# Optimization experiments

Measured on AMD Instinct MI355X. Metric: run time of the kernel, lower is better.

The kernel has to match this reference:

```python
import jax, jax.numpy as jnp
import numpy as np

B, C, H, W = 8, 256, 64, 64
OUT, K = 256, 3
OG = 1
STRIDE, PAD, DIL = 1, 1, 1
K2 = K * K


def setup_inputs() -> dict:
    key = jax.random.key(0)
    ks = jax.random.split(key, 5)
    x = jax.random.normal(ks[0], (B, C, H, W), jnp.float32)
    # main deform-conv weight [out, in//groups, k, k]
    weight = jax.random.normal(ks[1], (OUT, C, K, K), jnp.float32) * (1.0 / np.sqrt(C * K2))
    bias = jax.random.normal(ks[2], (OUT,), jnp.float32) * 0.01
    # param_generator: 3x3 conv -> 3*OG*K*K channels (oh, ow, mask)
    pg_w = jax.random.normal(ks[3], (3 * OG * K2, C, 3, 3), jnp.float32) * 0.01
    pg_b = jax.random.normal(ks[4], (3 * OG * K2,), jnp.float32) * 0.01
    return {"x": x, "weight": weight, "bias": bias, "pg_w": pg_w, "pg_b": pg_b}


def _conv3x3(x, w, b):
    y = jax.lax.conv_general_dilated(
        x, w, (1, 1), [(1, 1), (1, 1)],
        dimension_numbers=("NCHW", "OIHW", "NCHW"))
    return y + b[None, :, None, None]


def _bilinear_gather(img, py, px):
    # img [B,C,H,W]; py,px [B,K2,Ho,Wo] -> [B,C,K2,Ho,Wo]
    # Zero padding outside the image (torchvision deform_conv2d semantics).
    Hh, Ww = img.shape[2], img.shape[3]
    y0 = jnp.floor(py)
    x0 = jnp.floor(px)
    dy = py - y0
    dx = px - x0
    imgf = img.reshape(img.shape[0], img.shape[1], Hh * Ww)
    out = jnp.zeros((img.shape[0], img.shape[1]) + py.shape[1:], img.dtype)
    corners = (
        (0, 0, (1 - dy) * (1 - dx)),
        (0, 1, (1 - dy) * dx),
        (1, 0, dy * (1 - dx)),
        (1, 1, dy * dx),
    )
    for oy, ox, wgt in corners:
        yy = y0 + oy
        xx = x0 + ox
        valid = (yy >= 0) & (yy < Hh) & (xx >= 0) & (xx < Ww)
        yi = jnp.clip(yy, 0, Hh - 1).astype(jnp.int32)
        xi = jnp.clip(xx, 0, Ww - 1).astype(jnp.int32)
        idx = yi * Ww + xi  # [B,K2,Ho,Wo]
        g = jax.vmap(lambda im, ix: jnp.take(im, ix.reshape(-1), axis=1))(imgf, idx)
        g = g.reshape(img.shape[0], img.shape[1], *idx.shape[1:])
        out = out + g * (wgt * valid)[:, None]
    return out


def _deform_conv2d(x, weight, bias, pg_w, pg_b):
    Bn = x.shape[0]
    Hi, Wi = x.shape[2], x.shape[3]
    Ho = (Hi + 2 * PAD - DIL * (K - 1) - 1) // STRIDE + 1
    Wo = (Wi + 2 * PAD - DIL * (K - 1) - 1) // STRIDE + 1
    params = _conv3x3(x, pg_w, pg_b)  # [B, 3*OG*K2, H, W]
    oh, ow, mask = jnp.split(params, 3, axis=1)
    offset = jnp.concatenate([oh, ow], axis=1)  # [B, 2*OG*K2, Ho, Wo]
    mask = jax.nn.sigmoid(mask)                  # [B, OG*K2, Ho, Wo]
    # torchvision layout: channel = ((og*K2 + k)*2 + {y,x})
    off = offset.reshape(Bn, OG, K2, 2, Ho, Wo)
    dy = off[:, :, :, 0].reshape(Bn, K2, Ho, Wo)  # OG == 1
    dx = off[:, :, :, 1].reshape(Bn, K2, Ho, Wo)
    hy = jnp.arange(Ho, dtype=x.dtype) * STRIDE - PAD
    wx = jnp.arange(Wo, dtype=x.dtype) * STRIDE - PAD
    ky, kx = jnp.meshgrid(jnp.arange(K), jnp.arange(K), indexing="ij")
    base_y = hy[None, :, None] + (ky.reshape(-1) * DIL).astype(x.dtype)[:, None, None]  # [K2,Ho,1]
    base_x = wx[None, None, :] + (kx.reshape(-1) * DIL).astype(x.dtype)[:, None, None]  # [K2,1,Wo]
    py = dy + base_y[None]  # [B,K2,Ho,Wo]
    px = dx + base_x[None]
    sampled = _bilinear_gather(x, py, px)          # [B,C,K2,Ho,Wo]
    sampled = sampled * mask[:, None]              # modulation (OG=1)
    out = jnp.einsum("bckhw,ock->bohw", sampled, weight.reshape(OUT, C, K2))
    return out + bias[None, :, None, None]


def reference(x, weight, bias, pg_w, pg_b):
    return _deform_conv2d(x, weight, bias, pg_w, pg_b)
```

## Files before the change

### kernel.cpp

```cpp
#include <hip/hip_runtime.h>
#include <math.h>

#define BQ   8
#define CIN  256
#define HH   64
#define WW   64
#define COUT 256
#define K2   9
#define PCH  27

#define PT     64
#define CCH    32
#define NCHUNK (CIN / CCH)
#define NSTEP  72
#define NSUB   24
#define SUBROW 104
#define PLANE  (HH * WW)

#define NXT    (BQ * HH * 4)
#define NPW    ((NSTEP * COUT * 4) / 256)
#define NPG    ((NSTEP * 32 * 4) / 256)
#define NPREP  (NXT + NPW + NPG)

typedef __attribute__((ext_vector_type(8))) short short8;
typedef __attribute__((ext_vector_type(4))) float f32x4;
typedef __attribute__((ext_vector_type(2))) float f32x2;

#define PIPE_BARRIER() do {                                   \
    asm volatile("s_waitcnt lgkmcnt(0)" ::: "memory");        \
    __builtin_amdgcn_s_barrier();                             \
    asm volatile("" ::: "memory");                            \
} while (0)

static __device__ __forceinline__ unsigned short f2bf(float f) {
    unsigned u = __builtin_bit_cast(unsigned, f);
    u += 0x7fff + ((u >> 16) & 1);
    return (unsigned short)(u >> 16);
}
static __device__ __forceinline__ f32x2 up2(unsigned u) {
    f32x2 r;
    r[0] = __builtin_bit_cast(float, u << 16);
    r[1] = __builtin_bit_cast(float, u & 0xffff0000u);
    return r;
}
static __device__ __forceinline__ unsigned cvtpk(float lo, float hi) {
    unsigned r;
    asm("v_cvt_pk_bf16_f32 %0, %1, %2" : "=v"(r) : "v"(lo), "v"(hi));
    return r;
}

__global__ __launch_bounds__(256) void k_prep(const float* __restrict__ x,
                                              unsigned short* __restrict__ xT,
                                              const float* __restrict__ w,
                                              unsigned short* __restrict__ wp,
                                              const float* __restrict__ pgw,
                                              unsigned short* __restrict__ wpg) {
    __shared__ float tile[64][65];
    int blk = blockIdx.x;

    if (blk < NXT) {
        int cc  = blk & 3;
        int y   = (blk >> 2) & 63;
        int b   = blk >> 8;
        int t   = threadIdx.x;
        int c0  = cc * 64;

        const float* xp = x + ((size_t)(b * CIN + c0) * HH + y) * WW;
#pragma unroll
        for (int r = 0; r < 16; ++r) {
            int cl = r * 4 + (t >> 6);
            int xx = t & 63;
            tile[cl][xx] = xp[(size_t)cl * PLANE + xx];
        }
        __syncthreads();
        unsigned short* op = xT + ((size_t)b * PLANE + (size_t)y * WW) * CIN + c0;
#pragma unroll
        for (int r = 0; r < 16; ++r) {
            int xx = r * 4 + (t >> 6);
            int cl = t & 63;
            op[(size_t)xx * CIN + cl] = f2bf(tile[cl][xx]);
        }
    } else if (blk < NXT + NPW) {
        int t = (blk - NXT) * 256 + threadIdx.x;
        int q = t & 3;
        int o = (t >> 2) & 255;
        int s = t >> 10;
        short8 sv;
#pragma unroll
        for (int j = 0; j < 8; ++j) {
            int pos   = s * 32 + q * 8 + j;
            int chunk = pos / (CCH * K2);
            int pl    = pos % (CCH * K2);
            int ktap  = pl >> 5;
            int c     = chunk * CCH + (pl & 31);
            sv[j] = (short)f2bf(w[(o * CIN + c) * K2 + ktap]);
        }
        *(short8*)(wp + (size_t)t * 8) = sv;
    } else {
        int t = (blk - NXT - NPW) * 256 + threadIdx.x;
        int q = t & 3;
        int o = (t >> 2) & 31;
        int s = t >> 7;
        short8 sv;
#pragma unroll
        for (int j = 0; j < 8; ++j) {
            int pos   = s * 32 + q * 8 + j;
            int chunk = pos / (CCH * K2);
            int pl    = pos % (CCH * K2);
            int ktap  = pl >> 5;
            int c     = chunk * CCH + (pl & 31);
            sv[j] = (o < PCH) ? (short)f2bf(pgw[(size_t)(o * CIN + c) * K2 + ktap]) : (short)0;
        }
        *(short8*)(wpg + (size_t)t * 8) = sv;
    }
}

__global__ __launch_bounds__(512, 2) void k_params(const unsigned short* __restrict__ xT,
                                                   const unsigned short* __restrict__ wpg,
                                                   const float* __restrict__ pgb,
                                                   float* __restrict__ pv) {
    __shared__ alignas(16) unsigned short s_rows[2][3][66][40];

    int blk = blockIdx.x;
    int swz = (blk & 7) * 64 + (blk >> 3);
    int b   = swz >> 6;
    int h   = swz & 63;
    int t   = threadIdx.x;

    int wv  = t >> 6;
    int lm  = t & 15;
    int lq  = (t >> 4) & 3;
    int ipg = wv >> 2;
    int rpg = wv & 3;

    const unsigned short* xTb = xT + (size_t)b * PLANE * CIN;

    if (t < 48) {
        int bufk = t >= 24;
        int tt  = t - bufk * 24;
        int ky  = tt >> 3;
        int rem = tt & 7;
        int col = (rem >> 2) * 65;
        int q   = rem & 3;
        uint4 z = make_uint4(0, 0, 0, 0);
        *(uint4*)&s_rows[bufk][ky][col][q * 8] = z;
    }
    __syncthreads();

    f32x4 accA = (f32x4){0.f, 0.f, 0.f, 0.f};
    f32x4 accB = (f32x4){0.f, 0.f, 0.f, 0.f};

    int pxm1 = t >> 3;
    int cgs  = (t & 7) * 4;

    uint2 R[3];
#pragma unroll
    for (int ky = 0; ky < 3; ++ky) {
        int y = h + ky - 1;
        R[ky] = make_uint2(0, 0);
        if ((unsigned)y < (unsigned)HH)
            R[ky] = *(const uint2*)(xTb + (size_t)(y * WW + pxm1) * CIN + cgs);
    }

    for (int ch = 0; ch < NCHUNK; ++ch) {
#pragma unroll
        for (int ky = 0; ky < 3; ++ky)
            *(uint2*)&s_rows[ch & 1][ky][pxm1 + 1][cgs] = R[ky];
        if (ch + 1 < NCHUNK) {
#pragma unroll
            for (int ky = 0; ky < 3; ++ky) {
                int y = h + ky - 1;
                R[ky] = make_uint2(0, 0);
                if ((unsigned)y < (unsigned)HH)
                    R[ky] = *(const uint2*)(xTb + (size_t)(y * WW + pxm1) * CIN
                                            + (ch + 1) * CCH + cgs);
            }
        }
        __syncthreads();
#pragma unroll
        for (int tap = 0; tap < K2; ++tap) {
            int ky = tap / 3, kx = tap % 3;
            short8 a  = *(const short8*)(wpg + (size_t)(ch * K2 + tap) * 32 * 32
                                         + (ipg * 16 + lm) * 32 + lq * 8);
            short8 bf = *(const short8*)&s_rows[ch & 1][ky][rpg * 16 + lm + kx][lq * 8];
            if (tap & 1)
                accB = __builtin_amdgcn_mfma_f32_16x16x32_bf16(a, bf, accB, 0, 0, 0);
            else
                accA = __builtin_amdgcn_mfma_f32_16x16x32_bf16(a, bf, accA, 0, 0, 0);
        }
    }

    f32x4 accpg = accA + accB;
    int px = rpg * 16 + lm;
#pragma unroll
    for (int rg = 0; rg < 4; ++rg) {
        int oc = ipg * 16 + lq * 4 + rg;
        if (oc < PCH)
            pv[((size_t)(b * PCH + oc) << 12) + h * WW + px] = accpg[rg] + pgb[oc];
    }
}

__global__ __launch_bounds__(512, 4) void k_fused(const unsigned short* __restrict__ xT,
                                                  const unsigned short* __restrict__ wp,
                                                  const float* __restrict__ pv,
                                                  const float* __restrict__ bias,
                                                  float* __restrict__ out) {
    __shared__ alignas(16) unsigned short s_samp[2][PT][SUBROW];
    __shared__ float4 s_wgt4[K2][PT];
    __shared__ int4   s_off4[K2][PT];

    int blk = blockIdx.x;
    int swz = (blk & 7) * 64 + (blk >> 3);
    int b   = swz >> 6;
    int h   = swz & 63;
    int t   = threadIdx.x;

    int gp = t >> 3;
    int cg = t & 7;
    int wv = t >> 6;
    int lm = t & 15;
    int lq = (t >> 4) & 3;

    const char* xTb = (const char*)xT + (size_t)b * PLANE * CIN * 2;

    const float* pvb = pv + ((size_t)(b * PCH) << 12) + h * WW;
    for (int e = t; e < K2 * PT; e += 512) {
        int k = e >> 6;
        int p = e & 63;
        float dy = pvb[(size_t)(2 * k) << 12 | (unsigned)p];
        float dx = pvb[(size_t)(2 * k + 1) << 12 | (unsigned)p];
        float mz = pvb[(size_t)(18 + k) << 12 | (unsigned)p];
        float m  = 1.f / (1.f + expf(-mz));

        float py = dy + (float)(h - 1 + k / 3);
        float px = dx + (float)(p - 1 + k % 3);
        float y0f = floorf(py), x0f = floorf(px);
        float fy = py - y0f,    fx = px - x0f;
        int iy0 = (int)y0f, ix0 = (int)x0f;
        int iy1 = iy0 + 1,  ix1 = ix0 + 1;
        bool vy0 = (unsigned)iy0 < (unsigned)HH;
        bool vy1 = (unsigned)iy1 < (unsigned)HH;
        bool vx0 = (unsigned)ix0 < (unsigned)WW;
        bool vx1 = (unsigned)ix1 < (unsigned)WW;

        float w00 = (1.f - fy) * (1.f - fx) * m; if (!(vy0 && vx0)) w00 = 0.f;
        float w01 = (1.f - fy) * fx         * m; if (!(vy0 && vx1)) w01 = 0.f;
        float w10 = fy         * (1.f - fx) * m; if (!(vy1 && vx0)) w10 = 0.f;
        float w11 = fy         * fx         * m; if (!(vy1 && vx1)) w11 = 0.f;

        int cy0 = min(max(iy0, 0), HH - 1), cy1 = min(max(iy1, 0), HH - 1);
        int cx0 = min(max(ix0, 0), WW - 1), cx1 = min(max(ix1, 0), WW - 1);

        s_wgt4[k][p] = make_float4(w00, w01, w10, w11);
        s_off4[k][p] = make_int4((cy0 * WW + cx0) * 512, (cy0 * WW + cx1) * 512,
                                 (cy1 * WW + cx0) * 512, (cy1 * WW + cx1) * 512);
    }
    __syncthreads();

    int ow = wv * 32;
    f32x4 acc[2][4];
#pragma unroll
    for (int i = 0; i < 2; ++i)
#pragma unroll
        for (int j = 0; j < 4; ++j) acc[i][j] = (f32x4){0.f, 0.f, 0.f, 0.f};

    uint2 G[3][4];
    {
#pragma unroll
        for (int j = 0; j < 3; ++j) {
            int4 ob = s_off4[j][gp];
            G[j][0] = *(const uint2*)(xTb + ob.x + cg * 8);
            G[j][1] = *(const uint2*)(xTb + ob.y + cg * 8);
            G[j][2] = *(const uint2*)(xTb + ob.z + cg * 8);
            G[j][3] = *(const uint2*)(xTb + ob.w + cg * 8);
        }
#pragma unroll
        for (int j = 0; j < 3; ++j) {
            float4 gw = s_wgt4[j][gp];
            f32x2 v01 = gw.x * up2(G[j][0].x) + gw.y * up2(G[j][1].x)
                      + gw.z * up2(G[j][2].x) + gw.w * up2(G[j][3].x);
            f32x2 v23 = gw.x * up2(G[j][0].y) + gw.y * up2(G[j][1].y)
                      + gw.z * up2(G[j][2].y) + gw.w * up2(G[j][3].y);
            uint2 pk;
            pk.x = cvtpk(v01[0], v01[1]);
            pk.y = cvtpk(v23[0], v23[1]);
            *(uint2*)&s_samp[0][gp][j * 32 + cg * 4] = pk;
        }
#pragma unroll
        for (int j = 0; j < 3; ++j) {
            int4 ob = s_off4[3 + j][gp];
            G[j][0] = *(const uint2*)(xTb + ob.x + cg * 8);
            G[j][1] = *(const uint2*)(xTb + ob.y + cg * 8);
            G[j][2] = *(const uint2*)(xTb + ob.z + cg * 8);
            G[j][3] = *(const uint2*)(xTb + ob.w + cg * 8);
        }
        PIPE_BARRIER();
    }

    short8 a0c = *(const short8*)(wp + (ow +  0 + lm) * 32 + lq * 8);
    short8 a1c = *(const short8*)(wp + (ow + 16 + lm) * 32 + lq * 8);
    for (int sc = 0; sc < NSUB; ++sc) {
        bool doC = (sc + 1 < NSUB);
        bool doL = (sc + 2 < NSUB);
        int t1 = ((sc + 1) % 3) * 3;
        int t2 = ((sc + 2) % 3) * 3;
        int c2 = ((sc + 2) / 3) * (CCH * 2) + cg * 8;
        unsigned short (*__restrict__ bc)[SUBROW] = s_samp[sc & 1];
        unsigned short (*__restrict__ bn)[SUBROW] = s_samp[(sc + 1) & 1];
#pragma unroll
        for (int sl = 0; sl < 3; ++sl) {
            short8 b0 = *(const short8*)&bc[ 0 + lm][sl * 32 + lq * 8];
            short8 b1 = *(const short8*)&bc[16 + lm][sl * 32 + lq * 8];
            short8 b2 = *(const short8*)&bc[32 + lm][sl * 32 + lq * 8];
            short8 b3 = *(const short8*)&bc[48 + lm][sl * 32 + lq * 8];
            int r = sc * 3 + sl + 1;
            short8 a0n = a0c, a1n = a1c;
            if (r < NSTEP) {
                const unsigned short* wrn = wp + (size_t)r * COUT * 32;
                a0n = *(const short8*)(wrn + (ow +  0 + lm) * 32 + lq * 8);
                a1n = *(const short8*)(wrn + (ow + 16 + lm) * 32 + lq * 8);
            }
            if (doC) {
                float4 gw = s_wgt4[t1 + sl][gp];
                f32x2 v01 = gw.x * up2(G[sl][0].x) + gw.y * up2(G[sl][1].x)
                          + gw.z * up2(G[sl][2].x) + gw.w * up2(G[sl][3].x);
                f32x2 v23 = gw.x * up2(G[sl][0].y) + gw.y * up2(G[sl][1].y)
                          + gw.z * up2(G[sl][2].y) + gw.w * up2(G[sl][3].y);
                uint2 pk;
                pk.x = cvtpk(v01[0], v01[1]);
                pk.y = cvtpk(v23[0], v23[1]);
                *(uint2*)&bn[gp][sl * 32 + cg * 4] = pk;
            }
            if (doL) {
                int4 ob = s_off4[t2 + sl][gp];
                G[sl][0] = *(const uint2*)(xTb + ob.x + c2);
                G[sl][1] = *(const uint2*)(xTb + ob.y + c2);
                G[sl][2] = *(const uint2*)(xTb + ob.z + c2);
                G[sl][3] = *(const uint2*)(xTb + ob.w + c2);
            }
            __builtin_amdgcn_s_setprio(1);
            acc[0][0] = __builtin_amdgcn_mfma_f32_16x16x32_bf16(a0c, b0, acc[0][0], 0, 0, 0);
            acc[0][1] = __builtin_amdgcn_mfma_f32_16x16x32_bf16(a0c, b1, acc[0][1], 0, 0, 0);
            acc[0][2] = __builtin_amdgcn_mfma_f32_16x16x32_bf16(a0c, b2, acc[0][2], 0, 0, 0);
            acc[0][3] = __builtin_amdgcn_mfma_f32_16x16x32_bf16(a0c, b3, acc[0][3], 0, 0, 0);
            acc[1][0] = __builtin_amdgcn_mfma_f32_16x16x32_bf16(a1c, b0, acc[1][0], 0, 0, 0);
            acc[1][1] = __builtin_amdgcn_mfma_f32_16x16x32_bf16(a1c, b1, acc[1][1], 0, 0, 0);
            acc[1][2] = __builtin_amdgcn_mfma_f32_16x16x32_bf16(a1c, b2, acc[1][2], 0, 0, 0);
            acc[1][3] = __builtin_amdgcn_mfma_f32_16x16x32_bf16(a1c, b3, acc[1][3], 0, 0, 0);
            __builtin_amdgcn_s_setprio(0);
            a0c = a0n; a1c = a1n;
        }
        PIPE_BARRIER();
    }

    float* op = out + ((size_t)b * COUT) * PLANE + h * WW;
#pragma unroll
    for (int i = 0; i < 2; ++i) {
        int o0 = ow + i * 16 + lq * 4;
        f32x4 bv = *(const f32x4*)(bias + o0);
#pragma unroll
        for (int rg = 0; rg < 4; ++rg) {
#pragma unroll
            for (int j = 0; j < 4; ++j)
                op[(size_t)(o0 + rg) * PLANE + j * 16 + lm] = acc[i][j][rg] + bv[rg];
        }
    }
}

extern "C" void kernel_launch(void* const* d_in, const int* in_sizes, int n_in,
                              void* d_out, int out_size, void* d_ws, size_t ws_size,
                              hipStream_t stream) {
    const float* x    = (const float*)d_in[0];
    const float* wgt  = (const float*)d_in[1];
    const float* bias = (const float*)d_in[2];
    const float* pgw  = (const float*)d_in[3];
    const float* pgb  = (const float*)d_in[4];
    float* out = (float*)d_out;

    const size_t WPK_B = (size_t)NSTEP * COUT * 32 * 2;
    const size_t WPG_B = (size_t)NSTEP * 32 * 32 * 2;
    const size_t XT_B  = (size_t)BQ * PLANE * CIN * 2;
    unsigned short* wpk = (unsigned short*)d_ws;
    unsigned short* wpg = (unsigned short*)((char*)d_ws + WPK_B);
    unsigned short* xT  = (unsigned short*)((char*)d_ws + WPK_B + WPG_B);
    float*          pv  = (float*)((char*)d_ws + WPK_B + WPG_B + XT_B);

    k_prep  <<<NPREP, 256, 0, stream>>>(x, xT, wgt, wpk, pgw, wpg);
    k_params<<<BQ * HH, 512, 0, stream>>>(xT, wpg, pgb, pv);
    k_fused <<<BQ * HH, 512, 0, stream>>>(xT, wpk, pv, bias, out);
}
```

Before: 111.0 us.

## Merge offset-param conv into prep kernel reading fp32 x; retile fused MFMA warps

The offset/mask parameter convolution now runs inside the prep kernel, alongside the transpose and weight-packing blocks, and reads fp32 x directly with on-the-fly bf16 conversion. This removes the dependency on the transposed xT buffer and lets param work overlap with the transpose. The pg weight packing moves into a small separate kernel. In the fused kernel, each warp now covers 64 output channels by 32 pixels instead of 32 by 64, which changes the ratio of A-operand (weight) loads to B-operand LDS reads. The cost is more weight registers per warp, and the scalar LDS stores used for the in-kernel transpose may hit bank conflicts.

```diff
diff --git a/kernel.cpp b/kernel.cpp
--- a/kernel.cpp
+++ b/kernel.cpp
@@ -17,10 +17,10 @@
 #define SUBROW 104
 #define PLANE  (HH * WW)
 
+#define NPAR   512
 #define NXT    (BQ * HH * 4)
-#define NPW    ((NSTEP * COUT * 4) / 256)
-#define NPG    ((NSTEP * 32 * 4) / 256)
-#define NPREP  (NXT + NPW + NPG)
+#define NPW    ((NSTEP * COUT * 4) / 512)
+#define NPREP  (NPAR + NXT + NPW)
 
 typedef __attribute__((ext_vector_type(8))) short short8;
 typedef __attribute__((ext_vector_type(4))) float f32x4;
@@ -49,39 +49,141 @@
     return r;
 }
 
-__global__ __launch_bounds__(256) void k_prep(const float* __restrict__ x,
-                                              unsigned short* __restrict__ xT,
-                                              const float* __restrict__ w,
-                                              unsigned short* __restrict__ wp,
-                                              const float* __restrict__ pgw,
-                                              unsigned short* __restrict__ wpg) {
-    __shared__ float tile[64][65];
+__global__ __launch_bounds__(256) void k_pg(const float* __restrict__ pgw,
+                                            unsigned short* __restrict__ wpg) {
+    int t = blockIdx.x * 256 + threadIdx.x;
+    if (t >= NSTEP * 32 * 4) return;
+    int q = t & 3;
+    int o = (t >> 2) & 31;
+    int s = t >> 7;
+    short8 sv;
+#pragma unroll
+    for (int j = 0; j < 8; ++j) {
+        int pos   = s * 32 + q * 8 + j;
+        int chunk = pos / (CCH * K2);
+        int pl    = pos % (CCH * K2);
+        int ktap  = pl >> 5;
+        int c     = chunk * CCH + (pl & 31);
+        sv[j] = (o < PCH) ? (short)f2bf(pgw[(size_t)(o * CIN + c) * K2 + ktap]) : (short)0;
+    }
+    *(short8*)(wpg + (size_t)t * 8) = sv;
+}
+
+__global__ __launch_bounds__(512, 2) void k_prep(const float* __restrict__ x,
+                                                 unsigned short* __restrict__ xT,
+                                                 const float* __restrict__ w,
+                                                 unsigned short* __restrict__ wp,
+                                                 const unsigned short* __restrict__ wpg,
+                                                 const float* __restrict__ pgb,
+                                                 float* __restrict__ pv) {
+    __shared__ alignas(16) unsigned short smem[2][3][66][40];
     int blk = blockIdx.x;
-
-    if (blk < NXT) {
-        int cc  = blk & 3;
-        int y   = (blk >> 2) & 63;
-        int b   = blk >> 8;
-        int t   = threadIdx.x;
+    int tid = threadIdx.x;
+
+    if (blk < NPAR) {
+        int swz = (blk & 7) * 64 + (blk >> 3);
+        int b   = swz >> 6;
+        int h   = swz & 63;
+
+        int wv  = tid >> 6;
+        int lm  = tid & 15;
+        int lq  = (tid >> 4) & 3;
+        int ipg = wv >> 2;
+        int rpg = wv & 3;
+
+        if (tid < 48) {
+            int bufk = tid >= 24;
+            int tt  = tid - bufk * 24;
+            int ky  = tt >> 3;
+            int rem = tt & 7;
+            int col = (rem >> 2) * 65;
+            int q   = rem & 3;
+            uint4 z = make_uint4(0, 0, 0, 0);
+            *(uint4*)&smem[bufk][ky][col][q * 8] = z;
+        }
+        __syncthreads();
+
+        f32x4 accA = (f32x4){0.f, 0.f, 0.f, 0.f};
+        f32x4 accB = (f32x4){0.f, 0.f, 0.f, 0.f};
+
+        int cst = tid >> 4;
+        int px0 = (tid & 15) * 4;
+
+        const float* xb = x + (size_t)b * CIN * PLANE;
+
+        float4 R[3];
+#pragma unroll
+        for (int ky = 0; ky < 3; ++ky) {
+            int y = h + ky - 1;
+            R[ky] = make_float4(0.f, 0.f, 0.f, 0.f);
+            if ((unsigned)y < (unsigned)HH)
+                R[ky] = *(const float4*)(xb + ((size_t)cst * HH + y) * WW + px0);
+        }
+
+        for (int ch = 0; ch < NCHUNK; ++ch) {
+#pragma unroll
+            for (int ky = 0; ky < 3; ++ky) {
+                smem[ch & 1][ky][px0 + 1][cst] = f2bf(R[ky].x);
+                smem[ch & 1][ky][px0 + 2][cst] = f2bf(R[ky].y);
+                smem[ch & 1][ky][px0 + 3][cst] = f2bf(R[ky].z);
+                smem[ch & 1][ky][px0 + 4][cst] = f2bf(R[ky].w);
+            }
+            if (ch + 1 < NCHUNK) {
+#pragma unroll
+                for (int ky = 0; ky < 3; ++ky) {
+                    int y = h + ky - 1;
+                    R[ky] = make_float4(0.f, 0.f, 0.f, 0.f);
+                    if ((unsigned)y < (unsigned)HH)
+                        R[ky] = *(const float4*)(xb + ((size_t)((ch + 1) * CCH + cst) * HH + y) * WW + px0);
+                }
+            }
+            __syncthreads();
+#pragma unroll
+            for (int tap = 0; tap < K2; ++tap) {
+                int ky = tap / 3, kx = tap % 3;
+                short8 a  = *(const short8*)(wpg + (size_t)(ch * K2 + tap) * 32 * 32
+                                             + (ipg * 16 + lm) * 32 + lq * 8);
+                short8 bf = *(const short8*)&smem[ch & 1][ky][rpg * 16 + lm + kx][lq * 8];
+                if (tap & 1)
+                    accB = __builtin_amdgcn_mfma_f32_16x16x32_bf16(a, bf, accB, 0, 0, 0);
+                else
+                    accA = __builtin_amdgcn_mfma_f32_16x16x32_bf16(a, bf, accA, 0, 0, 0);
+            }
+        }
+
+        f32x4 accpg = accA + accB;
+        int px = rpg * 16 + lm;
+#pragma unroll
+        for (int rg = 0; rg < 4; ++rg) {
+            int oc = ipg * 16 + lq * 4 + rg;
+            if (oc < PCH)
+                pv[((size_t)(b * PCH + oc) << 12) + h * WW + px] = accpg[rg] + pgb[oc];
+        }
+    } else if (blk < NPAR + NXT) {
+        float (*tile)[65] = (float (*)[65])&smem[0][0][0][0];
+        int bb  = blk - NPAR;
+        int cc  = bb & 3;
+        int y   = (bb >> 2) & 63;
+        int b   = bb >> 8;
         int c0  = cc * 64;
 
         const float* xp = x + ((size_t)(b * CIN + c0) * HH + y) * WW;
 #pragma unroll
-        for (int r = 0; r < 16; ++r) {
-            int cl = r * 4 + (t >> 6);
-            int xx = t & 63;
+        for (int r = 0; r < 8; ++r) {
+            int cl = r * 8 + (tid >> 6);
+            int xx = tid & 63;
             tile[cl][xx] = xp[(size_t)cl * PLANE + xx];
         }
         __syncthreads();
         unsigned short* op = xT + ((size_t)b * PLANE + (size_t)y * WW) * CIN + c0;
 #pragma unroll
-        for (int r = 0; r < 16; ++r) {
-            int xx = r * 4 + (t >> 6);
-            int cl = t & 63;
+        for (int r = 0; r < 8; ++r) {
+            int xx = r * 8 + (tid >> 6);
+            int cl = tid & 63;
             op[(size_t)xx * CIN + cl] = f2bf(tile[cl][xx]);
         }
-    } else if (blk < NXT + NPW) {
-        int t = (blk - NXT) * 256 + threadIdx.x;
+    } else {
+        int t = (blk - NPAR - NXT) * 512 + tid;
         int q = t & 3;
         int o = (t >> 2) & 255;
         int s = t >> 10;
@@ -96,107 +198,6 @@
             sv[j] = (short)f2bf(w[(o * CIN + c) * K2 + ktap]);
         }
         *(short8*)(wp + (size_t)t * 8) = sv;
-    } else {
-        int t = (blk - NXT - NPW) * 256 + threadIdx.x;
-        int q = t & 3;
-        int o = (t >> 2) & 31;
-        int s = t >> 7;
-        short8 sv;
-#pragma unroll
-        for (int j = 0; j < 8; ++j) {
-            int pos   = s * 32 + q * 8 + j;
-            int chunk = pos / (CCH * K2);
-            int pl    = pos % (CCH * K2);
-            int ktap  = pl >> 5;
-            int c     = chunk * CCH + (pl & 31);
-            sv[j] = (o < PCH) ? (short)f2bf(pgw[(size_t)(o * CIN + c) * K2 + ktap]) : (short)0;
-        }
-        *(short8*)(wpg + (size_t)t * 8) = sv;
-    }
-}
-
-__global__ __launch_bounds__(512, 2) void k_params(const unsigned short* __restrict__ xT,
-                                                   const unsigned short* __restrict__ wpg,
-                                                   const float* __restrict__ pgb,
-                                                   float* __restrict__ pv) {
-    __shared__ alignas(16) unsigned short s_rows[2][3][66][40];
-
-    int blk = blockIdx.x;
-    int swz = (blk & 7) * 64 + (blk >> 3);
-    int b   = swz >> 6;
-    int h   = swz & 63;
-    int t   = threadIdx.x;
-
-    int wv  = t >> 6;
-    int lm  = t & 15;
-    int lq  = (t >> 4) & 3;
-    int ipg = wv >> 2;
-    int rpg = wv & 3;
-
-    const unsigned short* xTb = xT + (size_t)b * PLANE * CIN;
-
-    if (t < 48) {
-        int bufk = t >= 24;
-        int tt  = t - bufk * 24;
-        int ky  = tt >> 3;
-        int rem = tt & 7;
-        int col = (rem >> 2) * 65;
-        int q   = rem & 3;
-        uint4 z = make_uint4(0, 0, 0, 0);
-        *(uint4*)&s_rows[bufk][ky][col][q * 8] = z;
-    }
-    __syncthreads();
-
-    f32x4 accA = (f32x4){0.f, 0.f, 0.f, 0.f};
-    f32x4 accB = (f32x4){0.f, 0.f, 0.f, 0.f};
-
-    int pxm1 = t >> 3;
-    int cgs  = (t & 7) * 4;
-
-    uint2 R[3];
-#pragma unroll
-    for (int ky = 0; ky < 3; ++ky) {
-        int y = h + ky - 1;
-        R[ky] = make_uint2(0, 0);
-        if ((unsigned)y < (unsigned)HH)
-            R[ky] = *(const uint2*)(xTb + (size_t)(y * WW + pxm1) * CIN + cgs);
-    }
-
-    for (int ch = 0; ch < NCHUNK; ++ch) {
-#pragma unroll
-        for (int ky = 0; ky < 3; ++ky)
-            *(uint2*)&s_rows[ch & 1][ky][pxm1 + 1][cgs] = R[ky];
-        if (ch + 1 < NCHUNK) {
-#pragma unroll
-            for (int ky = 0; ky < 3; ++ky) {
-                int y = h + ky - 1;
-                R[ky] = make_uint2(0, 0);
-                if ((unsigned)y < (unsigned)HH)
-                    R[ky] = *(const uint2*)(xTb + (size_t)(y * WW + pxm1) * CIN
-                                            + (ch + 1) * CCH + cgs);
-            }
-        }
-        __syncthreads();
-#pragma unroll
-        for (int tap = 0; tap < K2; ++tap) {
-            int ky = tap / 3, kx = tap % 3;
-            short8 a  = *(const short8*)(wpg + (size_t)(ch * K2 + tap) * 32 * 32
-                                         + (ipg * 16 + lm) * 32 + lq * 8);
-            short8 bf = *(const short8*)&s_rows[ch & 1][ky][rpg * 16 + lm + kx][lq * 8];
-            if (tap & 1)
-                accB = __builtin_amdgcn_mfma_f32_16x16x32_bf16(a, bf, accB, 0, 0, 0);
-            else
-                accA = __builtin_amdgcn_mfma_f32_16x16x32_bf16(a, bf, accA, 0, 0, 0);
-        }
-    }
-
-    f32x4 accpg = accA + accB;
-    int px = rpg * 16 + lm;
-#pragma unroll
-    for (int rg = 0; rg < 4; ++rg) {
-        int oc = ipg * 16 + lq * 4 + rg;
-        if (oc < PCH)
-            pv[((size_t)(b * PCH + oc) << 12) + h * WW + px] = accpg[rg] + pgb[oc];
     }
 }
 
@@ -257,12 +258,13 @@
     }
     __syncthreads();
 
-    int ow = wv * 32;
-    f32x4 acc[2][4];
-#pragma unroll
-    for (int i = 0; i < 2; ++i)
-#pragma unroll
-        for (int j = 0; j < 4; ++j) acc[i][j] = (f32x4){0.f, 0.f, 0.f, 0.f};
+    int ow  = (wv >> 1) * 64;
+    int pxt = (wv & 1) * 32;
+    f32x4 acc[4][2];
+#pragma unroll
+    for (int i = 0; i < 4; ++i)
+#pragma unroll
+        for (int j = 0; j < 2; ++j) acc[i][j] = (f32x4){0.f, 0.f, 0.f, 0.f};
 
     uint2 G[3][4];
     {
@@ -297,8 +299,11 @@
         PIPE_BARRIER();
     }
 
-    short8 a0c = *(const short8*)(wp + (ow +  0 + lm) * 32 + lq * 8);
-    short8 a1c = *(const short8*)(wp + (ow + 16 + lm) * 32 + lq * 8);
+    short8 aC[4], aN[4];
+#pragma unroll
+    for (int i = 0; i < 4; ++i)
+        aC[i] = *(const short8*)(wp + (ow + i * 16 + lm) * 32 + lq * 8);
+
     for (int sc = 0; sc < NSUB; ++sc) {
         bool doC = (sc + 1 < NSUB);
         bool doL = (sc + 2 < NSUB);
@@ -309,16 +314,16 @@
         unsigned short (*__restrict__ bn)[SUBROW] = s_samp[(sc + 1) & 1];
 #pragma unroll
         for (int sl = 0; sl < 3; ++sl) {
-            short8 b0 = *(const short8*)&bc[ 0 + lm][sl * 32 + lq * 8];
-            short8 b1 = *(const short8*)&bc[16 + lm][sl * 32 + lq * 8];
-            short8 b2 = *(const short8*)&bc[32 + lm][sl * 32 + lq * 8];
-            short8 b3 = *(const short8*)&bc[48 + lm][sl * 32 + lq * 8];
+            short8 b0 = *(const short8*)&bc[pxt +  0 + lm][sl * 32 + lq * 8];
+            short8 b1 = *(const short8*)&bc[pxt + 16 + lm][sl * 32 + lq * 8];
             int r = sc * 3 + sl + 1;
-            short8 a0n = a0c, a1n = a1c;
+#pragma unroll
+            for (int i = 0; i < 4; ++i) aN[i] = aC[i];
             if (r < NSTEP) {
                 const unsigned short* wrn = wp + (size_t)r * COUT * 32;
-                a0n = *(const short8*)(wrn + (ow +  0 + lm) * 32 + lq * 8);
-                a1n = *(const short8*)(wrn + (ow + 16 + lm) * 32 + lq * 8);
+#pragma unroll
+                for (int i = 0; i < 4; ++i)
+                    aN[i] = *(const short8*)(wrn + (ow + i * 16 + lm) * 32 + lq * 8);
             }
             if (doC) {
                 float4 gw = s_wgt4[t1 + sl][gp];
@@ -339,29 +344,30 @@
                 G[sl][3] = *(const uint2*)(xTb + ob.w + c2);
             }
             __builtin_amdgcn_s_setprio(1);
-            acc[0][0] = __builtin_amdgcn_mfma_f32_16x16x32_bf16(a0c, b0, acc[0][0], 0, 0, 0);
-            acc[0][1] = __builtin_amdgcn_mfma_f32_16x16x32_bf16(a0c, b1, acc[0][1], 0, 0, 0);
-            acc[0][2] = __builtin_amdgcn_mfma_f32_16x16x32_bf16(a0c, b2, acc[0][2], 0, 0, 0);
-            acc[0][3] = __builtin_amdgcn_mfma_f32_16x16x32_bf16(a0c, b3, acc[0][3], 0, 0, 0);
-            acc[1][0] = __builtin_amdgcn_mfma_f32_16x16x32_bf16(a1c, b0, acc[1][0], 0, 0, 0);
-            acc[1][1] = __builtin_amdgcn_mfma_f32_16x16x32_bf16(a1c, b1, acc[1][1], 0, 0, 0);
-            acc[1][2] = __builtin_amdgcn_mfma_f32_16x16x32_bf16(a1c, b2, acc[1][2], 0, 0, 0);
-            acc[1][3] = __builtin_amdgcn_mfma_f32_16x16x32_bf16(a1c, b3, acc[1][3], 0, 0, 0);
+            acc[0][0] = __builtin_amdgcn_mfma_f32_16x16x32_bf16(aC[0], b0, acc[0][0], 0, 0, 0);
+            acc[0][1] = __builtin_amdgcn_mfma_f32_16x16x32_bf16(aC[0], b1, acc[0][1], 0, 0, 0);
+            acc[1][0] = __builtin_amdgcn_mfma_f32_16x16x32_bf16(aC[1], b0, acc[1][0], 0, 0, 0);
+            acc[1][1] = __builtin_amdgcn_mfma_f32_16x16x32_bf16(aC[1], b1, acc[1][1], 0, 0, 0);
+            acc[2][0] = __builtin_amdgcn_mfma_f32_16x16x32_bf16(aC[2], b0, acc[2][0], 0, 0, 0);
+            acc[2][1] = __builtin_amdgcn_mfma_f32_16x16x32_bf16(aC[2], b1, acc[2][1], 0, 0, 0);
+            acc[3][0] = __builtin_amdgcn_mfma_f32_16x16x32_bf16(aC[3], b0, acc[3][0], 0, 0, 0);
+            acc[3][1] = __builtin_amdgcn_mfma_f32_16x16x32_bf16(aC[3], b1, acc[3][1], 0, 0, 0);
             __builtin_amdgcn_s_setprio(0);
-            a0c = a0n; a1c = a1n;
+#pragma unroll
+            for (int i = 0; i < 4; ++i) aC[i] = aN[i];
         }
         PIPE_BARRIER();
     }
 
-    float* op = out + ((size_t)b * COUT) * PLANE + h * WW;
-#pragma unroll
-    for (int i = 0; i < 2; ++i) {
+    float* op = out + ((size_t)b * COUT) * PLANE + h * WW + pxt;
+#pragma unroll
+    for (int i = 0; i < 4; ++i) {
         int o0 = ow + i * 16 + lq * 4;
         f32x4 bv = *(const f32x4*)(bias + o0);
 #pragma unroll
         for (int rg = 0; rg < 4; ++rg) {
 #pragma unroll
-            for (int j = 0; j < 4; ++j)
+            for (int j = 0; j < 2; ++j)
                 op[(size_t)(o0 + rg) * PLANE + j * 16 + lm] = acc[i][j][rg] + bv[rg];
         }
     }
@@ -385,7 +391,7 @@
     unsigned short* xT  = (unsigned short*)((char*)d_ws + WPK_B + WPG_B);
     float*          pv  = (float*)((char*)d_ws + WPK_B + WPG_B + XT_B);
 
-    k_prep  <<<NPREP, 256, 0, stream>>>(x, xT, wgt, wpk, pgw, wpg);
-    k_params<<<BQ * HH, 512, 0, stream>>>(xT, wpg, pgb, pv);
-    k_fused <<<BQ * HH, 512, 0, stream>>>(xT, wpk, pv, bias, out);
-}
+    k_pg   <<<(NSTEP * 32 * 4 + 255) / 256, 256, 0, stream>>>(pgw, wpg);
+    k_prep <<<NPREP, 512, 0, stream>>>(x, xT, wgt, wpk, wpg, pgb, pv);
+    k_fused<<<BQ * HH, 512, 0, stream>>>(xT, wpk, pv, bias, out);
+}
```

Result: slower. 145.8 us (+31.4%).
